# Kernel tuning notes

Hardware: AMD Instinct MI355X
Metric: run time of the kernel (lower is better)

The kernel has to match this reference:

```python
import jax, jax.numpy as jnp
import numpy as np

B, C, N = 8, 128, 65536
NUM_OBJ = 64


def setup_inputs() -> dict:
    key = jax.random.key(0)
    k1, k2 = jax.random.split(key)
    point_features = jax.random.normal(k1, (B, C, N), dtype=jnp.float32)
    # box assignment per point (output of points_in_boxes_gpu in the original)
    box_idx = jax.random.randint(k2, (B, N), 0, NUM_OBJ, dtype=jnp.int64)
    return {"point_features": point_features, "box_idx": box_idx, "num_obj": NUM_OBJ}


def reference(point_features, box_idx, num_obj):
    # point_features: (B, C, N) float; box_idx: (B, N) int in [0, num_obj)
    b, c, n = point_features.shape
    # (B, N, C) -> (B*N, C): one feature row per point
    feats = jnp.transpose(point_features, (0, 2, 1)).reshape(b * n, c)
    # global segment id: batch-local boxes become distinct segments
    seg_ids = (jnp.arange(b, dtype=box_idx.dtype)[:, None] * num_obj + box_idx).reshape(-1)
    # fused gather + segment max (replaces per-box max_pool1d python loop)
    seg_max = jax.ops.segment_max(feats, seg_ids, num_segments=b * num_obj)
    # guard (empty segments -> -inf); original assumes nonempty boxes
    seg_max = jnp.where(jnp.isfinite(seg_max), seg_max, jnp.zeros_like(seg_max))
    return seg_max  # (B*num_obj, C) == pretext_head_feats
```

## Files before the change

### kernel.cpp

```cpp
#include <hip/hip_runtime.h>
#include <cstdint>
#include <cstddef>

#define BATCH 8
#define CH    128
#define NPTS  65536
#define NOBJ  64
#define TPB   256
#define SEGEL (CH * NOBJ)

__device__ __forceinline__ uint32_t enc_f32(float f) {
    uint32_t x = __float_as_uint(f);
    return x ^ ((uint32_t)((int32_t)x >> 31) | 0x80000000u);
}
__device__ __forceinline__ float dec_f32(uint32_t u) {
    uint32_t x = u ^ ((uint32_t)((int32_t)(~u) >> 31) | 0x80000000u);
    return __uint_as_float(x);
}

template <int NCHUNK>
__global__ __launch_bounds__(TPB) void seg_max_ws(
        const float* __restrict__ pf,
        const int*   __restrict__ bidx,
        uint32_t*    __restrict__ ws)
{
    constexpr int PPB = NPTS / NCHUNK;
    constexpr int J   = PPB / 4 / 32;
    static_assert(J >= 1, "chunk too small");

    __shared__ uint32_t acc[SEGEL];

    const int tid  = threadIdx.x;
    const int wave = tid >> 6;
    const int lane = tid & 63;
    const int cl   = lane >> 3;
    const int pq   = lane & 7;

    const int b     = blockIdx.x / NCHUNK;
    const int chunk = blockIdx.x % NCHUNK;
    const int n0    = chunk * PPB;

    for (int i = tid; i < SEGEL; i += TPB) acc[i] = 0u;

    int s[J][4];
    #pragma unroll
    for (int j = 0; j < J; ++j) {
        const int q = j * 32 + wave * 8 + pq;
        const int4 sv = *(const int4*)(bidx + (size_t)b * NPTS + n0 + q * 4);
        s[j][0] = sv.x ^ cl;  s[j][1] = sv.y ^ cl;
        s[j][2] = sv.z ^ cl;  s[j][3] = sv.w ^ cl;
    }
    __syncthreads();

    const float* pbase = pf + (size_t)b * CH * NPTS + n0;
    const int qoff = (wave * 8 + pq) * 4;

    float4 v[J], vn[J];
    {
        const float* pc = pbase + (size_t)cl * NPTS;
        #pragma unroll
        for (int j = 0; j < J; ++j) v[j] = *(const float4*)(pc + j * 128 + qoff);
    }

    for (int cb = 0; cb < CH; cb += 8) {
        if (cb + 8 < CH) {
            const float* pn = pbase + (size_t)(cb + 8 + cl) * NPTS;
            #pragma unroll
            for (int j = 0; j < J; ++j) vn[j] = *(const float4*)(pn + j * 128 + qoff);
        }
        uint32_t* row = acc + (cb + cl) * NOBJ;
        #pragma unroll
        for (int j = 0; j < J; ++j) {
            atomicMax(&row[s[j][0]], enc_f32(v[j].x));
            atomicMax(&row[s[j][1]], enc_f32(v[j].y));
            atomicMax(&row[s[j][2]], enc_f32(v[j].z));
            atomicMax(&row[s[j][3]], enc_f32(v[j].w));
        }
        #pragma unroll
        for (int j = 0; j < J; ++j) v[j] = vn[j];
    }
    __syncthreads();

    uint32_t* wsb = ws + (size_t)blockIdx.x * SEGEL;
    for (int e = tid; e < SEGEL; e += TPB) wsb[e] = acc[e];
}

template <int NCHUNK>
__global__ __launch_bounds__(256) void reduce_ws(
        const uint32_t* __restrict__ ws, float* __restrict__ out)
{
    const int g = blockIdx.x * 256 + threadIdx.x;
    const int b = g >> 13;
    const int e = g & (SEGEL - 1);
    const uint32_t* p = ws + (size_t)b * NCHUNK * SEGEL + e;
    uint32_t m = 0u;
    #pragma unroll
    for (int k = 0; k < NCHUNK; ++k) m = max(m, p[(size_t)k * SEGEL]);
    const int c   = e >> 6;
    const int seg = (e & 63) ^ (c & 7);
    float f = 0.0f;
    if (m) { f = dec_f32(m); if (!isfinite(f)) f = 0.0f; }
    out[(size_t)(b * NOBJ + seg) * CH + c] = f;
}

__global__ __launch_bounds__(256) void init_out_kernel(uint32_t* __restrict__ out, int n) {
    int i = blockIdx.x * blockDim.x + threadIdx.x;
    if (i < n) out[i] = 0u;
}

__global__ __launch_bounds__(TPB) void seg_max_atomic(
        const float* __restrict__ pf, const int* __restrict__ bidx,
        uint32_t* __restrict__ out)
{
    constexpr int PPB = 1024;
    __shared__ uint32_t acc[SEGEL];
    const int tid   = threadIdx.x;
    const int b     = blockIdx.x / (NPTS / PPB);
    const int chunk = blockIdx.x % (NPTS / PPB);
    const int n0    = chunk * PPB;
    for (int i = tid; i < SEGEL; i += TPB) acc[i] = 0u;
    __syncthreads();
    const int4 sv = *(const int4*)(bidx + (size_t)b * NPTS + n0 + tid * 4);
    const float* p = pf + (size_t)b * CH * NPTS + n0 + tid * 4;
    uint32_t* row = acc;
    #pragma unroll 4
    for (int c = 0; c < CH; ++c, p += NPTS, row += NOBJ) {
        const float4 v = *(const float4*)p;
        atomicMax(&row[sv.x], enc_f32(v.x));
        atomicMax(&row[sv.y], enc_f32(v.y));
        atomicMax(&row[sv.z], enc_f32(v.z));
        atomicMax(&row[sv.w], enc_f32(v.w));
    }
    __syncthreads();
    for (int e = tid; e < SEGEL; e += TPB) {
        const int seg = e & (NOBJ - 1);
        const int c   = e >> 6;
        const uint32_t v = acc[c * NOBJ + seg];
        if (v) atomicMax(&out[(size_t)(b * NOBJ + seg) * CH + c], v);
    }
}

__global__ __launch_bounds__(256) void finalize_kernel(uint32_t* __restrict__ out, int n) {
    int i = blockIdx.x * blockDim.x + threadIdx.x;
    if (i >= n) return;
    const uint32_t u = out[i];
    float f = 0.0f;
    if (u) { f = dec_f32(u); if (!isfinite(f)) f = 0.0f; }
    ((float*)out)[i] = f;
}

extern "C" void kernel_launch(void* const* d_in, const int* in_sizes, int n_in,
                              void* d_out, int out_size, void* d_ws, size_t ws_size,
                              hipStream_t stream) {
    const float* pf   = (const float*)d_in[0];
    const int*   bidx = (const int*)d_in[1];

    const size_t need128 = (size_t)BATCH * 128 * SEGEL * 4;
    const size_t need64  = (size_t)BATCH *  64 * SEGEL * 4;

    if (ws_size >= need128) {
        uint32_t* ws = (uint32_t*)d_ws;
        seg_max_ws<128><<<BATCH * 128, TPB, 0, stream>>>(pf, bidx, ws);
        reduce_ws<128><<<(BATCH * SEGEL) / 256, 256, 0, stream>>>(ws, (float*)d_out);
    } else if (ws_size >= need64) {
        uint32_t* ws = (uint32_t*)d_ws;
        seg_max_ws<64><<<BATCH * 64, TPB, 0, stream>>>(pf, bidx, ws);
        reduce_ws<64><<<(BATCH * SEGEL) / 256, 256, 0, stream>>>(ws, (float*)d_out);
    } else {
        uint32_t* out = (uint32_t*)d_out;
        init_out_kernel<<<(out_size + 255) / 256, 256, 0, stream>>>(out, out_size);
        seg_max_atomic<<<BATCH * (NPTS / 1024), TPB, 0, stream>>>(pf, bidx, out);
        finalize_kernel<<<(out_size + 255) / 256, 256, 0, stream>>>(out, out_size);
    }
}
```

Before: 367.8 us.

## Replace per-point LDS atomics with counting-sort and segmented max reduction

```diff
diff --git a/kernel.cpp b/kernel.cpp
--- a/kernel.cpp
+++ b/kernel.cpp
@@ -6,8 +6,12 @@
 #define CH    128
 #define NPTS  65536
 #define NOBJ  64
-#define TPB   256
 #define SEGEL (CH * NOBJ)
+
+#define TPB2  512
+#define PPB2  1024
+#define NCH2  (NPTS / PPB2)
+#define WSL   1152
 
 __device__ __forceinline__ uint32_t enc_f32(float f) {
     uint32_t x = __float_as_uint(f);
@@ -18,71 +22,128 @@
     return __uint_as_float(x);
 }
 
-template <int NCHUNK>
-__global__ __launch_bounds__(TPB) void seg_max_ws(
+__global__ __launch_bounds__(TPB2) void seg_max_sort(
         const float* __restrict__ pf,
         const int*   __restrict__ bidx,
         uint32_t*    __restrict__ ws)
 {
-    constexpr int PPB = NPTS / NCHUNK;
-    constexpr int J   = PPB / 4 / 32;
-    static_assert(J >= 1, "chunk too small");
-
-    __shared__ uint32_t acc[SEGEL];
-
-    const int tid  = threadIdx.x;
-    const int wave = tid >> 6;
-    const int lane = tid & 63;
-    const int cl   = lane >> 3;
-    const int pq   = lane & 7;
-
-    const int b     = blockIdx.x / NCHUNK;
-    const int chunk = blockIdx.x % NCHUNK;
-    const int n0    = chunk * PPB;
-
-    for (int i = tid; i < SEGEL; i += TPB) acc[i] = 0u;
-
-    int s[J][4];
-    #pragma unroll
-    for (int j = 0; j < J; ++j) {
-        const int q = j * 32 + wave * 8 + pq;
-        const int4 sv = *(const int4*)(bidx + (size_t)b * NPTS + n0 + q * 4);
-        s[j][0] = sv.x ^ cl;  s[j][1] = sv.y ^ cl;
-        s[j][2] = sv.z ^ cl;  s[j][3] = sv.w ^ cl;
-    }
-    __syncthreads();
+    __shared__ float    wavebuf[8 * WSL];
+    __shared__ uint32_t dest[PPB2];
+    __shared__ uint32_t slotseg[PPB2];
+    __shared__ uint32_t cnt[NOBJ];
+    __shared__ uint32_t off[NOBJ];
+    __shared__ uint32_t accbuf[8 * NOBJ];
+
+    const int tid = threadIdx.x;
+    const int w   = tid >> 6;
+    const int l   = tid & 63;
+    const int b     = blockIdx.x / NCH2;
+    const int chunk = blockIdx.x % NCH2;
+    const int n0    = chunk * PPB2;
+
+    if (tid < NOBJ) cnt[tid] = 0u;
+    __syncthreads();
+    const int2 sv = *(const int2*)(bidx + (size_t)b * NPTS + n0 + tid * 2);
+    const uint32_t r0 = atomicAdd(&cnt[sv.x], 1u);
+    const uint32_t r1 = atomicAdd(&cnt[sv.y], 1u);
+    __syncthreads();
+
+    if (tid < 64) {
+        const uint32_t c = cnt[tid];
+        uint32_t inc = c;
+        #pragma unroll
+        for (int d = 1; d < 64; d <<= 1) {
+            const uint32_t t = __shfl_up(inc, d, 64);
+            if (tid >= d) inc += t;
+        }
+        off[tid] = inc - c;
+    }
+    __syncthreads();
+
+    const uint32_t d0 = off[sv.x] + r0;
+    const uint32_t d1 = off[sv.y] + r1;
+    dest[tid * 2]     = d0;
+    dest[tid * 2 + 1] = d1;
+    slotseg[d0] = (uint32_t)sv.x;
+    slotseg[d1] = (uint32_t)sv.y;
+    __syncthreads();
+
+    uint32_t pdest[16];
+    #pragma unroll
+    for (int j = 0; j < 4; ++j) {
+        const uint4 dd = *(const uint4*)&dest[j * 256 + l * 4];
+        pdest[j * 4 + 0] = dd.x + (dd.x >> 3);
+        pdest[j * 4 + 1] = dd.y + (dd.y >> 3);
+        pdest[j * 4 + 2] = dd.z + (dd.z >> 3);
+        pdest[j * 4 + 3] = dd.w + (dd.w >> 3);
+    }
+    uint32_t seg16[16];
+    #pragma unroll
+    for (int j = 0; j < 4; ++j) {
+        const uint4 ss = *(const uint4*)&slotseg[l * 16 + j * 4];
+        seg16[j * 4 + 0] = ss.x;  seg16[j * 4 + 1] = ss.y;
+        seg16[j * 4 + 2] = ss.z;  seg16[j * 4 + 3] = ss.w;
+    }
+    uint32_t mask = 0x8000u;
+    #pragma unroll
+    for (int j = 0; j < 15; ++j)
+        mask |= (seg16[j] != seg16[j + 1] ? 1u : 0u) << j;
+    uint32_t wsp[4];
+    #pragma unroll
+    for (int q = 0; q < 4; ++q)
+        wsp[q] = seg16[q*4] | (seg16[q*4+1] << 8) | (seg16[q*4+2] << 16) | (seg16[q*4+3] << 24);
 
     const float* pbase = pf + (size_t)b * CH * NPTS + n0;
-    const int qoff = (wave * 8 + pq) * 4;
-
-    float4 v[J], vn[J];
+    float*    bw  = wavebuf + w * WSL;
+    uint32_t* acc = accbuf + w * NOBJ;
+    uint32_t* wsb = ws + (size_t)blockIdx.x * SEGEL;
+
+    float4 v[4], vn[4];
     {
-        const float* pc = pbase + (size_t)cl * NPTS;
-        #pragma unroll
-        for (int j = 0; j < J; ++j) v[j] = *(const float4*)(pc + j * 128 + qoff);
+        const float* pc = pbase + (size_t)w * NPTS;
+        #pragma unroll
+        for (int j = 0; j < 4; ++j) v[j] = *(const float4*)(pc + j * 256 + l * 4);
     }
 
     for (int cb = 0; cb < CH; cb += 8) {
-        if (cb + 8 < CH) {
-            const float* pn = pbase + (size_t)(cb + 8 + cl) * NPTS;
+        const int c = cb + w;
+        const bool more = (cb + 8 < CH);
+        if (more) {
+            const float* pn = pbase + (size_t)(c + 8) * NPTS;
             #pragma unroll
-            for (int j = 0; j < J; ++j) vn[j] = *(const float4*)(pn + j * 128 + qoff);
-        }
-        uint32_t* row = acc + (cb + cl) * NOBJ;
-        #pragma unroll
-        for (int j = 0; j < J; ++j) {
-            atomicMax(&row[s[j][0]], enc_f32(v[j].x));
-            atomicMax(&row[s[j][1]], enc_f32(v[j].y));
-            atomicMax(&row[s[j][2]], enc_f32(v[j].z));
-            atomicMax(&row[s[j][3]], enc_f32(v[j].w));
-        }
-        #pragma unroll
-        for (int j = 0; j < J; ++j) v[j] = vn[j];
-    }
-    __syncthreads();
-
-    uint32_t* wsb = ws + (size_t)blockIdx.x * SEGEL;
-    for (int e = tid; e < SEGEL; e += TPB) wsb[e] = acc[e];
+            for (int j = 0; j < 4; ++j) vn[j] = *(const float4*)(pn + j * 256 + l * 4);
+        }
+
+        acc[l] = 0u;
+
+        #pragma unroll
+        for (int j = 0; j < 4; ++j) {
+            bw[pdest[j * 4 + 0]] = v[j].x;
+            bw[pdest[j * 4 + 1]] = v[j].y;
+            bw[pdest[j * 4 + 2]] = v[j].z;
+            bw[pdest[j * 4 + 3]] = v[j].w;
+        }
+
+        const int base = l * 18;
+        float m = -INFINITY;
+        #pragma unroll
+        for (int j = 0; j < 16; ++j) {
+            const float x = bw[base + j + (j >> 3)];
+            m = fmaxf(m, x);
+            if ((mask >> j) & 1u) {
+                const uint32_t seg = (wsp[j >> 2] >> ((j & 3) * 8)) & 0xFFu;
+                atomicMax(&acc[seg], enc_f32(m));
+                m = -INFINITY;
+            }
+        }
+
+        wsb[(size_t)c * NOBJ + l] = acc[l];
+
+        if (more) {
+            #pragma unroll
+            for (int j = 0; j < 4; ++j) v[j] = vn[j];
+        }
+    }
 }
 
 template <int NCHUNK>
@@ -97,7 +158,7 @@
     #pragma unroll
     for (int k = 0; k < NCHUNK; ++k) m = max(m, p[(size_t)k * SEGEL]);
     const int c   = e >> 6;
-    const int seg = (e & 63) ^ (c & 7);
+    const int seg = e & 63;
     float f = 0.0f;
     if (m) { f = dec_f32(m); if (!isfinite(f)) f = 0.0f; }
     out[(size_t)(b * NOBJ + seg) * CH + c] = f;
@@ -108,7 +169,7 @@
     if (i < n) out[i] = 0u;
 }
 
-__global__ __launch_bounds__(TPB) void seg_max_atomic(
+__global__ __launch_bounds__(256) void seg_max_atomic(
         const float* __restrict__ pf, const int* __restrict__ bidx,
         uint32_t* __restrict__ out)
 {
@@ -118,7 +179,7 @@
     const int b     = blockIdx.x / (NPTS / PPB);
     const int chunk = blockIdx.x % (NPTS / PPB);
     const int n0    = chunk * PPB;
-    for (int i = tid; i < SEGEL; i += TPB) acc[i] = 0u;
+    for (int i = tid; i < SEGEL; i += 256) acc[i] = 0u;
     __syncthreads();
     const int4 sv = *(const int4*)(bidx + (size_t)b * NPTS + n0 + tid * 4);
     const float* p = pf + (size_t)b * CH * NPTS + n0 + tid * 4;
@@ -132,7 +193,7 @@
         atomicMax(&row[sv.w], enc_f32(v.w));
     }
     __syncthreads();
-    for (int e = tid; e < SEGEL; e += TPB) {
+    for (int e = tid; e < SEGEL; e += 256) {
         const int seg = e & (NOBJ - 1);
         const int c   = e >> 6;
         const uint32_t v = acc[c * NOBJ + seg];
@@ -155,21 +216,16 @@
     const float* pf   = (const float*)d_in[0];
     const int*   bidx = (const int*)d_in[1];
 
-    const size_t need128 = (size_t)BATCH * 128 * SEGEL * 4;
-    const size_t need64  = (size_t)BATCH *  64 * SEGEL * 4;
-
-    if (ws_size >= need128) {
+    const size_t need = (size_t)BATCH * NCH2 * SEGEL * 4;
+
+    if (ws_size >= need) {
         uint32_t* ws = (uint32_t*)d_ws;
-        seg_max_ws<128><<<BATCH * 128, TPB, 0, stream>>>(pf, bidx, ws);
-        reduce_ws<128><<<(BATCH * SEGEL) / 256, 256, 0, stream>>>(ws, (float*)d_out);
-    } else if (ws_size >= need64) {
-        uint32_t* ws = (uint32_t*)d_ws;
-        seg_max_ws<64><<<BATCH * 64, TPB, 0, stream>>>(pf, bidx, ws);
-        reduce_ws<64><<<(BATCH * SEGEL) / 256, 256, 0, stream>>>(ws, (float*)d_out);
+        seg_max_sort<<<BATCH * NCH2, TPB2, 0, stream>>>(pf, bidx, ws);
+        reduce_ws<NCH2><<<(BATCH * SEGEL) / 256, 256, 0, stream>>>(ws, (float*)d_out);
     } else {
         uint32_t* out = (uint32_t*)d_out;
         init_out_kernel<<<(out_size + 255) / 256, 256, 0, stream>>>(out, out_size);
-        seg_max_atomic<<<BATCH * (NPTS / 1024), TPB, 0, stream>>>(pf, bidx, out);
+        seg_max_atomic<<<BATCH * (NPTS / 1024), 256, 0, stream>>>(pf, bidx, out);
         finalize_kernel<<<(out_size + 255) / 256, 256, 0, stream>>>(out, out_size);
     }
 }
```

Result: no change. 374.0 us (+1.7%).
